# Kernel optimization log

Measured on AMD Instinct MI355X. Metric: run time of the kernel, lower is better.

## Reference

```python
import jax, jax.numpy as jnp
import numpy as np

B, S, D, H = 2, 2048, 2048, 16
HD = D // H  # 128


def _rope(t, cos, sin):
    # t: [B, S, H, HD]; cos/sin: [S, HD//2]
    te, to = t[..., ::2], t[..., 1::2]
    c = cos[None, :, None, :]
    s = sin[None, :, None, :]
    re = te * c - to * s
    im = te * s + to * c
    # interleave back (matches tf.stack(..., axis=-1) + reshape)
    return jnp.stack([re, im], axis=-1).reshape(t.shape)


def setup_inputs() -> dict:
    key = jax.random.key(0)
    ks = jax.random.split(key, 6)
    x = jax.random.normal(ks[0], (B, S, D), dtype=jnp.float32)
    Wq = jax.random.normal(ks[1], (D, D), dtype=jnp.float32) * 0.02
    Wk = jax.random.normal(ks[2], (D, D), dtype=jnp.float32) * 0.02
    Wv = jax.random.normal(ks[3], (D, D), dtype=jnp.float32) * 0.02
    Wo = jax.random.normal(ks[4], (D, D), dtype=jnp.float32) * 0.02
    # rotary embeddings: freqs_cis = exp(i * pos * inv_freq)
    inv_freq = 1.0 / (10000.0 ** (jnp.arange(0, HD, 2, dtype=jnp.float32) / HD))  # [HD//2]
    angles = jnp.arange(S, dtype=jnp.float32)[:, None] * inv_freq[None, :]  # [S, HD//2]
    freqs_cos = jnp.cos(angles)
    freqs_sin = jnp.sin(angles)
    # additive causal mask [1,1,S,S]
    causal = jnp.tril(jnp.ones((S, S), dtype=bool))
    mask = jnp.where(causal, 0.0, -1e9).astype(jnp.float32)[None, None]
    return {"x": x, "Wq": Wq, "Wk": Wk, "Wv": Wv, "Wo": Wo,
            "freqs_cos": freqs_cos, "freqs_sin": freqs_sin, "mask": mask}


def reference(x, Wq, Wk, Wv, Wo, freqs_cos, freqs_sin, mask):
    b, s, d = x.shape
    xq = (x @ Wq).reshape(b, s, H, HD)
    xk = (x @ Wk).reshape(b, s, H, HD)
    xv = (x @ Wv).reshape(b, s, H, HD)
    xq = _rope(xq, freqs_cos, freqs_sin)
    xk = _rope(xk, freqs_cos, freqs_sin)
    # [B, H, S, HD]
    xq = xq.transpose(0, 2, 1, 3)
    xk = xk.transpose(0, 2, 1, 3)
    xv = xv.transpose(0, 2, 1, 3)
    scores = jnp.einsum('bhqd,bhkd->bhqk', xq, xk) / jnp.sqrt(jnp.float32(HD))
    scores = scores + mask[:, :, :s, :s]
    probs = jax.nn.softmax(scores + 1e-9, axis=-1)
    out = jnp.einsum('bhqk,bhkd->bhqd', probs, xv)
    out = out.transpose(0, 2, 1, 3).reshape(b, s, d)
    return out @ Wo
```

## Files before the change

### kernel.cpp

```cpp
#include <hip/hip_runtime.h>
#include <cstdint>

#define BB 2
#define SS 2048
#define DD 2048
#define HH 16
#define HDIM 128
#define MM (BB * SS)

typedef __attribute__((ext_vector_type(8))) short bf16x8;
typedef __attribute__((ext_vector_type(4))) short bf16x4;
typedef __attribute__((ext_vector_type(4))) float f32x4;
typedef __attribute__((ext_vector_type(16))) float f32x16;

__device__ inline short f2bf(float f) {
  union { float f; unsigned u; } v; v.f = f;
  unsigned r = v.u + 0x7FFFu + ((v.u >> 16) & 1u);
  return (short)(r >> 16);
}
__device__ inline float bf2f(short s) {
  union { float f; unsigned u; } v;
  v.u = ((unsigned)(unsigned short)s) << 16;
  return v.f;
}
__device__ inline float asf(int u) { union { int i; float f; } v; v.i = u; return v.f; }
__device__ inline int asi(float f) { union { float f; int i; } v; v.f = f; return v.i; }

__device__ inline unsigned cvtpk_bf16(float lo, float hi) {
  unsigned r;
  asm("v_cvt_pk_bf16_f32 %0, %1, %2" : "=v"(r) : "v"(lo), "v"(hi));
  return r;
}

__device__ inline void gll16(const void* g, void* l) {
  __builtin_amdgcn_global_load_lds(
      (const __attribute__((address_space(1))) void*)g,
      (__attribute__((address_space(3))) void*)l, 16, 0, 0);
}

__global__ __launch_bounds__(256) void cast_bf16_kernel(
    const float* __restrict__ x, short* __restrict__ y, int n4) {
  int i = blockIdx.x * 256 + threadIdx.x;
  if (i >= n4) return;
  float4 v = reinterpret_cast<const float4*>(x)[i];
  bf16x4 o;
  o[0] = f2bf(v.x); o[1] = f2bf(v.y); o[2] = f2bf(v.z); o[3] = f2bf(v.w);
  reinterpret_cast<bf16x4*>(y)[i] = o;
}

__global__ __launch_bounds__(256) void transpose_cast_kernel(
    const float* __restrict__ W, short* __restrict__ Wt) {
  __shared__ short tile[64][65];
  int c = threadIdx.x & 63, r4 = threadIdx.x >> 6;
  int n0 = blockIdx.x << 6, k0 = blockIdx.y << 6;
#pragma unroll
  for (int p = 0; p < 16; ++p) {
    int r = (p << 2) + r4;
    tile[c][r] = f2bf(W[(size_t)(k0 + r) * DD + n0 + c]);
  }
  __syncthreads();
#pragma unroll
  for (int p = 0; p < 16; ++p) {
    int r = (p << 2) + r4;
    Wt[(size_t)(n0 + r) * DD + k0 + c] = tile[r][c];
  }
}

__global__ __launch_bounds__(256) void transpose_v_kernel(
    const short* __restrict__ V, short* __restrict__ Vt) {
  __shared__ short tile[64][65];
  int c = threadIdx.x & 63, r4 = threadIdx.x >> 6;
  int s0 = blockIdx.x << 6, d0 = blockIdx.y << 6;
  int bh = blockIdx.z;
  int b = bh >> 4, h = bh & 15;
#pragma unroll
  for (int p = 0; p < 16; ++p) {
    int r = (p << 2) + r4;
    tile[c][r] = V[(size_t)(b * SS + s0 + r) * DD + h * HDIM + d0 + c];
  }
  __syncthreads();
#pragma unroll
  for (int p = 0; p < 16; ++p) {
    int r = (p << 2) + r4;
    Vt[((size_t)bh * HDIM + d0 + r) * SS + s0 + c] = tile[r][c];
  }
}

__global__ __launch_bounds__(256) void rope_kernel(
    short* __restrict__ Q, short* __restrict__ K,
    const float* __restrict__ fc, const float* __restrict__ fs) {
  int idx = blockIdx.x * 256 + threadIdx.x;
  int m = idx >> 8;
  int c8 = idx & 255;
  int s = m & (SS - 1);
  int i0 = (c8 & 15) << 2;
  const float QS = 0.08838834764831845f;
  float4 c4 = *reinterpret_cast<const float4*>(&fc[s * 64 + i0]);
  float4 s4 = *reinterpret_cast<const float4*>(&fs[s * 64 + i0]);
  float cc[4] = {c4.x, c4.y, c4.z, c4.w};
  float sn[4] = {s4.x, s4.y, s4.z, s4.w};
  size_t off = (size_t)m * DD + (c8 << 3);
  {
    bf16x8 v = *reinterpret_cast<bf16x8*>(&Q[off]);
    bf16x8 o;
#pragma unroll
    for (int p = 0; p < 4; ++p) {
      float e = bf2f(v[2 * p]), od = bf2f(v[2 * p + 1]);
      o[2 * p] = f2bf((e * cc[p] - od * sn[p]) * QS);
      o[2 * p + 1] = f2bf((e * sn[p] + od * cc[p]) * QS);
    }
    *reinterpret_cast<bf16x8*>(&Q[off]) = o;
  }
  {
    bf16x8 v = *reinterpret_cast<bf16x8*>(&K[off]);
    bf16x8 o;
#pragma unroll
    for (int p = 0; p < 4; ++p) {
      float e = bf2f(v[2 * p]), od = bf2f(v[2 * p + 1]);
      o[2 * p] = f2bf(e * cc[p] - od * sn[p]);
      o[2 * p + 1] = f2bf(e * sn[p] + od * cc[p]);
    }
    *reinterpret_cast<bf16x8*>(&K[off]) = o;
  }
}

template <typename OT>
__global__ __launch_bounds__(256) void gemm_kernel(
    const short* __restrict__ A, const short* __restrict__ Bt, OT* __restrict__ C,
    int Mdim, int Ndim, int Kdim) {
  __shared__ short As[128 * 64];
  __shared__ short Bs[128 * 64];
  int tid = threadIdx.x;
  int lane = tid & 63, w = tid >> 6;
  int cl = lane & 15, gq = lane >> 4;
  int wm = w >> 1, wn = w & 1;
  int m0 = blockIdx.y << 7, n0 = blockIdx.x << 7;
  f32x4 acc[4][4];
#pragma unroll
  for (int i = 0; i < 4; ++i)
#pragma unroll
    for (int j = 0; j < 4; ++j) {
      f32x4 z = {0.f, 0.f, 0.f, 0.f};
      acc[i][j] = z;
    }
  int lrow = lane >> 3;
  int lseg = (lane & 7) ^ lrow;

  for (int k0 = 0; k0 < Kdim; k0 += 64) {
#pragma unroll
    for (int i = 0; i < 4; ++i) {
      int r0 = ((w << 2) + i) << 3;
      gll16(&A[(size_t)(m0 + r0 + lrow) * Kdim + k0 + (lseg << 3)], &As[r0 << 6]);
      gll16(&Bt[(size_t)(n0 + r0 + lrow) * Kdim + k0 + (lseg << 3)], &Bs[r0 << 6]);
    }
    __syncthreads();
#pragma unroll
    for (int ks = 0; ks < 2; ++ks) {
      bf16x8 af[4], bfr[4];
#pragma unroll
      for (int f = 0; f < 4; ++f) {
        int ra = (wm << 6) + (f << 4) + cl;
        af[f] = *reinterpret_cast<const bf16x8*>(
            &As[((ra << 6) + (ks << 5) + (gq << 3)) ^ ((ra & 7) << 3)]);
        int rb = (wn << 6) + (f << 4) + cl;
        bfr[f] = *reinterpret_cast<const bf16x8*>(
            &Bs[((rb << 6) + (ks << 5) + (gq << 3)) ^ ((rb & 7) << 3)]);
      }
#pragma unroll
      for (int fm = 0; fm < 4; ++fm)
#pragma unroll
        for (int fn = 0; fn < 4; ++fn)
          acc[fm][fn] = __builtin_amdgcn_mfma_f32_16x16x32_bf16(
              af[fm], bfr[fn], acc[fm][fn], 0, 0, 0);
    }
    __syncthreads();
  }
#pragma unroll
  for (int fm = 0; fm < 4; ++fm)
#pragma unroll
    for (int r = 0; r < 4; ++r) {
      int mrow = m0 + (wm << 6) + (fm << 4) + (gq << 2) + r;
#pragma unroll
      for (int fn = 0; fn < 4; ++fn) {
        int ncol = n0 + (wn << 6) + (fn << 4) + cl;
        float vv = acc[fm][fn][r];
        if constexpr (sizeof(OT) == 2)
          C[(size_t)mrow * Ndim + ncol] = (OT)f2bf(vv);
        else
          C[(size_t)mrow * Ndim + ncol] = vv;
      }
    }
}

__global__ __launch_bounds__(256, 2) void attn_kernel(
    const short* __restrict__ Q, const short* __restrict__ K,
    const short* __restrict__ Vt, short* __restrict__ O) {
  __shared__ short Kl[2][64 * 128];
  __shared__ short Vl[2][128 * 64];
  const int id = blockIdx.x;
  const int qi = 15 - (id >> 5);
  const int bh = id & 31;
  const int b = bh >> 4, h = bh & 15;
  const int tid = threadIdx.x;
  const int lane = tid & 63, w = tid >> 6;
  const int l31 = lane & 31, hi = lane >> 5;
  const int qw = qi * 128 + w * 32;
  const int qg = qw + l31;

  const short* Kbase = K + (size_t)b * SS * DD + h * HDIM;
  const short* Vbase = Vt + (size_t)bh * HDIM * SS;
  int krow[4], kq[4], vd[4], vs[4];
#pragma unroll
  for (int i = 0; i < 4; ++i) {
    int c = w * 4 + i;
    krow[i] = c * 4 + (lane >> 4);
    kq[i] = (lane & 15) ^ (krow[i] & 7);
    vd[i] = c * 8 + (lane >> 3);
    vs[i] = (lane & 7) ^ (vd[i] & 7);
  }

  bf16x8 qf[8];
  const size_t qoff = ((size_t)b * SS + qg) * DD + h * HDIM;
#pragma unroll
  for (int s = 0; s < 8; ++s)
    qf[s] = *reinterpret_cast<const bf16x8*>(&Q[qoff + s * 16 + hi * 8]);

  f32x16 ot[4];
#pragma unroll
  for (int dt = 0; dt < 4; ++dt)
#pragma unroll
    for (int r = 0; r < 16; ++r) ot[dt][r] = 0.f;
  float m_run = -INFINITY, l_run = 0.f;

  const int NT = 2 * qi + 2;

#pragma unroll
  for (int i = 0; i < 4; ++i) {
    gll16(Kbase + (size_t)krow[i] * DD + kq[i] * 8, &Kl[0][(w * 4 + i) * 512]);
    gll16(Vbase + (size_t)vd[i] * SS + vs[i] * 8, &Vl[0][(w * 4 + i) * 512]);
  }
  __syncthreads();

  for (int t = 0; t < NT; ++t) {
    const int cur = t & 1;
    if (t + 1 < NT) {
      const int nt64 = (t + 1) * 64;
#pragma unroll
      for (int i = 0; i < 4; ++i) {
        gll16(Kbase + (size_t)(nt64 + krow[i]) * DD + kq[i] * 8,
              &Kl[cur ^ 1][(w * 4 + i) * 512]);
        gll16(Vbase + (size_t)vd[i] * SS + nt64 + vs[i] * 8,
              &Vl[cur ^ 1][(w * 4 + i) * 512]);
      }
    }

    if (t * 64 <= qw + 31) {
      const short* Kc = Kl[cur];
      const short* Vc = Vl[cur];
      f32x16 st0, st1;
#pragma unroll
      for (int r = 0; r < 16; ++r) { st0[r] = 0.f; st1[r] = 0.f; }
      __builtin_amdgcn_s_setprio(1);
#pragma unroll
      for (int s = 0; s < 8; ++s) {
        const int cs = (s * 2 + hi);
        bf16x8 kf0 = *reinterpret_cast<const bf16x8*>(
            &Kc[l31 * 128 + ((cs ^ (l31 & 7)) << 3)]);
        st0 = __builtin_amdgcn_mfma_f32_32x32x16_bf16(kf0, qf[s], st0, 0, 0, 0);
        bf16x8 kf1 = *reinterpret_cast<const bf16x8*>(
            &Kc[(32 + l31) * 128 + ((cs ^ (l31 & 7)) << 3)]);
        st1 = __builtin_amdgcn_mfma_f32_32x32x16_bf16(kf1, qf[s], st1, 0, 0, 0);
      }
      __builtin_amdgcn_s_setprio(0);
      if (t * 64 + 63 > qw) {
#pragma unroll
        for (int r = 0; r < 16; ++r) {
          int dl = (r & 3) + 8 * (r >> 2) + 4 * hi;
          if (t * 64 + dl > qg) st0[r] = -1e30f;
          if (t * 64 + 32 + dl > qg) st1[r] = -1e30f;
        }
      }
      float pm = st0[0];
#pragma unroll
      for (int r = 1; r < 16; ++r) pm = fmaxf(pm, st0[r]);
#pragma unroll
      for (int r = 0; r < 16; ++r) pm = fmaxf(pm, st1[r]);
      {
        auto sw = __builtin_amdgcn_permlane32_swap(asi(pm), asi(pm), false, false);
        pm = fmaxf(asf(sw[0]), asf(sw[1]));
      }
      if (!__all(pm <= m_run + 8.f)) {
        float mn = fmaxf(m_run, pm);
        float al = __expf(m_run - mn);
        m_run = mn;
        l_run *= al;
#pragma unroll
        for (int dt = 0; dt < 4; ++dt)
#pragma unroll
          for (int r = 0; r < 16; ++r) ot[dt][r] *= al;
      }
      float ps = 0.f;
#pragma unroll
      for (int r = 0; r < 16; ++r) { st0[r] = __expf(st0[r] - m_run); ps += st0[r]; }
#pragma unroll
      for (int r = 0; r < 16; ++r) { st1[r] = __expf(st1[r] - m_run); ps += st1[r]; }
      {
        auto sw = __builtin_amdgcn_permlane32_swap(asi(ps), asi(ps), false, false);
        ps = asf(sw[0]) + asf(sw[1]);
      }
      l_run += ps;

      bf16x8 pf[4];
#pragma unroll
      for (int s = 0; s < 4; ++s) {
        float e0, e1, e2, e3, e4, e5, e6, e7;
        if (s < 2) {
          e0 = st0[8 * s + 0]; e1 = st0[8 * s + 1]; e2 = st0[8 * s + 2]; e3 = st0[8 * s + 3];
          e4 = st0[8 * s + 4]; e5 = st0[8 * s + 5]; e6 = st0[8 * s + 6]; e7 = st0[8 * s + 7];
        } else {
          e0 = st1[8 * (s - 2) + 0]; e1 = st1[8 * (s - 2) + 1]; e2 = st1[8 * (s - 2) + 2]; e3 = st1[8 * (s - 2) + 3];
          e4 = st1[8 * (s - 2) + 4]; e5 = st1[8 * (s - 2) + 5]; e6 = st1[8 * (s - 2) + 6]; e7 = st1[8 * (s - 2) + 7];
        }
        unsigned a0 = cvtpk_bf16(e0, e1);
        unsigned a1 = cvtpk_bf16(e2, e3);
        unsigned b0 = cvtpk_bf16(e4, e5);
        unsigned b1 = cvtpk_bf16(e6, e7);
        auto r0 = __builtin_amdgcn_permlane32_swap((int)a0, (int)b0, false, false);
        auto r1 = __builtin_amdgcn_permlane32_swap((int)a1, (int)b1, false, false);
        union { int u[4]; bf16x8 v; } pk;
        pk.u[0] = r0[0]; pk.u[1] = r1[0]; pk.u[2] = r0[1]; pk.u[3] = r1[1];
        pf[s] = pk.v;
      }

      __builtin_amdgcn_s_setprio(1);
#pragma unroll
      for (int dt = 0; dt < 4; ++dt) {
        const int vr = dt * 32 + l31;
#pragma unroll
        for (int s = 0; s < 4; ++s) {
          bf16x8 vf = *reinterpret_cast<const bf16x8*>(
              &Vc[vr * 64 + (((s * 2 + hi) ^ (vr & 7)) << 3)]);
          ot[dt] = __builtin_amdgcn_mfma_f32_32x32x16_bf16(vf, pf[s], ot[dt], 0, 0, 0);
        }
      }
      __builtin_amdgcn_s_setprio(0);
    }
    __syncthreads();
  }

  float inv = 1.0f / l_run;
  const size_t orow = ((size_t)b * SS + qg) * DD + h * HDIM;
#pragma unroll
  for (int dt = 0; dt < 4; ++dt)
#pragma unroll
    for (int g = 0; g < 4; ++g) {
      bf16x4 v;
#pragma unroll
      for (int k = 0; k < 4; ++k) v[k] = f2bf(ot[dt][4 * g + k] * inv);
      *reinterpret_cast<bf16x4*>(&O[orow + dt * 32 + 8 * g + 4 * hi]) = v;
    }
}

extern "C" void kernel_launch(void* const* d_in, const int* in_sizes, int n_in,
                              void* d_out, int out_size, void* d_ws, size_t ws_size,
                              hipStream_t stream) {
  const float* x = (const float*)d_in[0];
  const float* Wq = (const float*)d_in[1];
  const float* Wk = (const float*)d_in[2];
  const float* Wv = (const float*)d_in[3];
  const float* Wo = (const float*)d_in[4];
  const float* fc = (const float*)d_in[5];
  const float* fs = (const float*)d_in[6];
  float* out = (float*)d_out;
  char* ws = (char*)d_ws;

  short* xb  = (short*)(ws + 0);
  short* WqT = (short*)(ws + (size_t)16 * 1048576);
  short* WkT = (short*)(ws + (size_t)24 * 1048576);
  short* WvT = (short*)(ws + (size_t)32 * 1048576);
  short* WoT = (short*)(ws + (size_t)40 * 1048576);
  short* Qb  = (short*)(ws + (size_t)48 * 1048576);
  short* Kb  = (short*)(ws + (size_t)64 * 1048576);
  short* Vb  = (short*)(ws + (size_t)80 * 1048576);

  cast_bf16_kernel<<<8192, 256, 0, stream>>>(x, xb, 2097152);
  dim3 tg(32, 32);
  transpose_cast_kernel<<<tg, 256, 0, stream>>>(Wq, WqT);
  transpose_cast_kernel<<<tg, 256, 0, stream>>>(Wk, WkT);
  transpose_cast_kernel<<<tg, 256, 0, stream>>>(Wv, WvT);
  transpose_cast_kernel<<<tg, 256, 0, stream>>>(Wo, WoT);

  dim3 gg(16, 32);
  gemm_kernel<short><<<gg, 256, 0, stream>>>(xb, WqT, Qb, MM, DD, DD);
  gemm_kernel<short><<<gg, 256, 0, stream>>>(xb, WkT, Kb, MM, DD, DD);
  gemm_kernel<short><<<gg, 256, 0, stream>>>(xb, WvT, Vb, MM, DD, DD);

  rope_kernel<<<4096, 256, 0, stream>>>(Qb, Kb, fc, fs);
  transpose_v_kernel<<<dim3(32, 2, 32), 256, 0, stream>>>(Vb, xb);

  attn_kernel<<<512, 256, 0, stream>>>(Qb, Kb, xb, Vb);

  gemm_kernel<float><<<gg, 256, 0, stream>>>(Vb, WoT, out, MM, DD, DD);
}
```

Before: 293.5 us.

## Fuse QKV projections with RoPE and V transpose into one GEMM; exp2 softmax

Concatenates Wq/Wk/Wv into one weight buffer and runs a single QKV GEMM whose epilogue applies RoPE (with the softmax scale folded into Q as log2e/sqrt(d)) and writes V already transposed through shared memory. This removes the separate rope and transpose kernels and their round trips through global memory, and fills the grid better with a single 1536-block launch. Attention switches to exp2 and uses tree reductions for the row max and sum, and raises the rescale threshold to 11.5 in the log2 domain, which roughly matches the old threshold of 8.

Measured after the change: 282.6 us. 3.7% less time.

```diff
diff --git a/kernel.cpp b/kernel.cpp
--- a/kernel.cpp
+++ b/kernel.cpp
@@ -66,67 +66,108 @@
   }
 }
 
-__global__ __launch_bounds__(256) void transpose_v_kernel(
-    const short* __restrict__ V, short* __restrict__ Vt) {
-  __shared__ short tile[64][65];
-  int c = threadIdx.x & 63, r4 = threadIdx.x >> 6;
-  int s0 = blockIdx.x << 6, d0 = blockIdx.y << 6;
-  int bh = blockIdx.z;
-  int b = bh >> 4, h = bh & 15;
-#pragma unroll
-  for (int p = 0; p < 16; ++p) {
-    int r = (p << 2) + r4;
-    tile[c][r] = V[(size_t)(b * SS + s0 + r) * DD + h * HDIM + d0 + c];
-  }
-  __syncthreads();
-#pragma unroll
-  for (int p = 0; p < 16; ++p) {
-    int r = (p << 2) + r4;
-    Vt[((size_t)bh * HDIM + d0 + r) * SS + s0 + c] = tile[r][c];
-  }
-}
-
-__global__ __launch_bounds__(256) void rope_kernel(
-    short* __restrict__ Q, short* __restrict__ K,
+__global__ __launch_bounds__(256) void qkv_gemm_kernel(
+    const short* __restrict__ A, const short* __restrict__ Bt,
+    short* __restrict__ Qb, short* __restrict__ Kb, short* __restrict__ Vt,
     const float* __restrict__ fc, const float* __restrict__ fs) {
-  int idx = blockIdx.x * 256 + threadIdx.x;
-  int m = idx >> 8;
-  int c8 = idx & 255;
-  int s = m & (SS - 1);
-  int i0 = (c8 & 15) << 2;
-  const float QS = 0.08838834764831845f;
-  float4 c4 = *reinterpret_cast<const float4*>(&fc[s * 64 + i0]);
-  float4 s4 = *reinterpret_cast<const float4*>(&fs[s * 64 + i0]);
-  float cc[4] = {c4.x, c4.y, c4.z, c4.w};
-  float sn[4] = {s4.x, s4.y, s4.z, s4.w};
-  size_t off = (size_t)m * DD + (c8 << 3);
-  {
-    bf16x8 v = *reinterpret_cast<bf16x8*>(&Q[off]);
-    bf16x8 o;
-#pragma unroll
-    for (int p = 0; p < 4; ++p) {
-      float e = bf2f(v[2 * p]), od = bf2f(v[2 * p + 1]);
-      o[2 * p] = f2bf((e * cc[p] - od * sn[p]) * QS);
-      o[2 * p + 1] = f2bf((e * sn[p] + od * cc[p]) * QS);
-    }
-    *reinterpret_cast<bf16x8*>(&Q[off]) = o;
-  }
-  {
-    bf16x8 v = *reinterpret_cast<bf16x8*>(&K[off]);
-    bf16x8 o;
-#pragma unroll
-    for (int p = 0; p < 4; ++p) {
-      float e = bf2f(v[2 * p]), od = bf2f(v[2 * p + 1]);
-      o[2 * p] = f2bf(e * cc[p] - od * sn[p]);
-      o[2 * p + 1] = f2bf(e * sn[p] + od * cc[p]);
-    }
-    *reinterpret_cast<bf16x8*>(&K[off]) = o;
-  }
-}
-
-template <typename OT>
+  __shared__ short smem[128 * 136];
+  short* As = smem;
+  short* Bs = smem + 8192;
+  const int tid = threadIdx.x;
+  const int lane = tid & 63, w = tid >> 6;
+  const int cl = lane & 15, gq = lane >> 4;
+  const int wm = w >> 1, wn = w & 1;
+  const int m0 = blockIdx.y << 7, n0 = blockIdx.x << 7;
+  const int mat = n0 >> 11;
+  f32x4 acc[4][4];
+#pragma unroll
+  for (int i = 0; i < 4; ++i)
+#pragma unroll
+    for (int j = 0; j < 4; ++j) {
+      f32x4 z = {0.f, 0.f, 0.f, 0.f};
+      acc[i][j] = z;
+    }
+  const int lrow = lane >> 3;
+  const int lseg = (lane & 7) ^ lrow;
+
+  for (int k0 = 0; k0 < DD; k0 += 64) {
+#pragma unroll
+    for (int i = 0; i < 4; ++i) {
+      int r0 = ((w << 2) + i) << 3;
+      gll16(&A[(size_t)(m0 + r0 + lrow) * DD + k0 + (lseg << 3)], &As[r0 << 6]);
+      gll16(&Bt[(size_t)(n0 + r0 + lrow) * DD + k0 + (lseg << 3)], &Bs[r0 << 6]);
+    }
+    __syncthreads();
+#pragma unroll
+    for (int ks = 0; ks < 2; ++ks) {
+      bf16x8 af[4], bfr[4];
+#pragma unroll
+      for (int f = 0; f < 4; ++f) {
+        int ra = (wm << 6) + (f << 4) + cl;
+        af[f] = *reinterpret_cast<const bf16x8*>(
+            &As[((ra << 6) + (ks << 5) + (gq << 3)) ^ ((ra & 7) << 3)]);
+        int rb = (wn << 6) + (f << 4) + cl;
+        bfr[f] = *reinterpret_cast<const bf16x8*>(
+            &Bs[((rb << 6) + (ks << 5) + (gq << 3)) ^ ((rb & 7) << 3)]);
+      }
+#pragma unroll
+      for (int fm = 0; fm < 4; ++fm)
+#pragma unroll
+        for (int fn = 0; fn < 4; ++fn)
+          acc[fm][fn] = __builtin_amdgcn_mfma_f32_16x16x32_bf16(
+              af[fm], bfr[fn], acc[fm][fn], 0, 0, 0);
+    }
+    __syncthreads();
+  }
+
+  if (mat < 2) {
+    const float qs = (mat == 0) ? 0.127517448f : 1.0f;
+    short* Dst = (mat == 0) ? Qb : Kb;
+#pragma unroll
+    for (int fm = 0; fm < 4; ++fm)
+#pragma unroll
+      for (int r = 0; r < 4; ++r) {
+        int mrow = m0 + (wm << 6) + (fm << 4) + (gq << 2) + r;
+        int s = mrow & (SS - 1);
+#pragma unroll
+        for (int fn = 0; fn < 4; ++fn) {
+          int c = (wn << 6) + (fn << 4) + cl;
+          int i = c >> 1;
+          float cv = fc[s * 64 + i], sv = fs[s * 64 + i];
+          float v = acc[fm][fn][r];
+          float vp = __shfl_xor(v, 1, 64);
+          float out = (c & 1) ? (v * cv + vp * sv) : (v * cv - vp * sv);
+          Dst[(size_t)mrow * DD + ((n0 + c) & (DD - 1))] = f2bf(out * qs);
+        }
+      }
+  } else {
+    short* Tt = smem;
+#pragma unroll
+    for (int fm = 0; fm < 4; ++fm)
+#pragma unroll
+      for (int fn = 0; fn < 4; ++fn) {
+        int c = (wn << 6) + (fn << 4) + cl;
+        int rb = (wm << 6) + (fm << 4) + (gq << 2);
+        bf16x4 v4;
+#pragma unroll
+        for (int rr = 0; rr < 4; ++rr) v4[rr] = f2bf(acc[fm][fn][rr]);
+        *reinterpret_cast<bf16x4*>(&Tt[c * 136 + rb]) = v4;
+      }
+    __syncthreads();
+    int d = tid >> 1, half = tid & 1;
+    int bq = m0 >> 11, s0loc = m0 & (SS - 1);
+    int hv = (n0 >> 7) - 32;
+    size_t vb = (((size_t)(bq * 16 + hv) * HDIM + d) * SS) + s0loc + half * 64;
+#pragma unroll
+    for (int j = 0; j < 8; ++j) {
+      bf16x8 v = *reinterpret_cast<const bf16x8*>(&Tt[d * 136 + half * 64 + j * 8]);
+      *reinterpret_cast<bf16x8*>(&Vt[vb + j * 8]) = v;
+    }
+  }
+}
+
 __global__ __launch_bounds__(256) void gemm_kernel(
-    const short* __restrict__ A, const short* __restrict__ Bt, OT* __restrict__ C,
+    const short* __restrict__ A, const short* __restrict__ Bt, float* __restrict__ C,
     int Mdim, int Ndim, int Kdim) {
   __shared__ short As[128 * 64];
   __shared__ short Bs[128 * 64];
@@ -183,11 +224,7 @@
 #pragma unroll
       for (int fn = 0; fn < 4; ++fn) {
         int ncol = n0 + (wn << 6) + (fn << 4) + cl;
-        float vv = acc[fm][fn][r];
-        if constexpr (sizeof(OT) == 2)
-          C[(size_t)mrow * Ndim + ncol] = (OT)f2bf(vv);
-        else
-          C[(size_t)mrow * Ndim + ncol] = vv;
+        C[(size_t)mrow * Ndim + ncol] = acc[fm][fn][r];
       }
     }
 }
@@ -280,18 +317,22 @@
           if (t * 64 + 32 + dl > qg) st1[r] = -1e30f;
         }
       }
-      float pm = st0[0];
-#pragma unroll
-      for (int r = 1; r < 16; ++r) pm = fmaxf(pm, st0[r]);
-#pragma unroll
-      for (int r = 0; r < 16; ++r) pm = fmaxf(pm, st1[r]);
+      float mx[16];
+#pragma unroll
+      for (int r = 0; r < 16; ++r) mx[r] = fmaxf(st0[r], st1[r]);
+#pragma unroll
+      for (int off = 8; off >= 1; off >>= 1)
+#pragma unroll
+        for (int r = 0; r < 8; ++r)
+          if (r < off) mx[r] = fmaxf(mx[r], mx[r + off]);
+      float pm = mx[0];
       {
         auto sw = __builtin_amdgcn_permlane32_swap(asi(pm), asi(pm), false, false);
         pm = fmaxf(asf(sw[0]), asf(sw[1]));
       }
-      if (!__all(pm <= m_run + 8.f)) {
+      if (!__all(pm <= m_run + 11.5f)) {
         float mn = fmaxf(m_run, pm);
-        float al = __expf(m_run - mn);
+        float al = exp2f(m_run - mn);
         m_run = mn;
         l_run *= al;
 #pragma unroll
@@ -299,11 +340,19 @@
 #pragma unroll
           for (int r = 0; r < 16; ++r) ot[dt][r] *= al;
       }
-      float ps = 0.f;
-#pragma unroll
-      for (int r = 0; r < 16; ++r) { st0[r] = __expf(st0[r] - m_run); ps += st0[r]; }
-#pragma unroll
-      for (int r = 0; r < 16; ++r) { st1[r] = __expf(st1[r] - m_run); ps += st1[r]; }
+#pragma unroll
+      for (int r = 0; r < 16; ++r) st0[r] = exp2f(st0[r] - m_run);
+#pragma unroll
+      for (int r = 0; r < 16; ++r) st1[r] = exp2f(st1[r] - m_run);
+      float sm[16];
+#pragma unroll
+      for (int r = 0; r < 16; ++r) sm[r] = st0[r] + st1[r];
+#pragma unroll
+      for (int off = 8; off >= 1; off >>= 1)
+#pragma unroll
+        for (int r = 0; r < 8; ++r)
+          if (r < off) sm[r] += sm[r + off];
+      float ps = sm[0];
       {
         auto sw = __builtin_amdgcn_permlane32_swap(asi(ps), asi(ps), false, false);
         ps = asf(sw[0]) + asf(sw[1]);
@@ -374,31 +423,23 @@
   float* out = (float*)d_out;
   char* ws = (char*)d_ws;
 
-  short* xb  = (short*)(ws + 0);
-  short* WqT = (short*)(ws + (size_t)16 * 1048576);
-  short* WkT = (short*)(ws + (size_t)24 * 1048576);
-  short* WvT = (short*)(ws + (size_t)32 * 1048576);
-  short* WoT = (short*)(ws + (size_t)40 * 1048576);
-  short* Qb  = (short*)(ws + (size_t)48 * 1048576);
-  short* Kb  = (short*)(ws + (size_t)64 * 1048576);
-  short* Vb  = (short*)(ws + (size_t)80 * 1048576);
+  short* xb     = (short*)(ws + 0);
+  short* WqkvT  = (short*)(ws + (size_t)16 * 1048576);
+  short* WoT    = (short*)(ws + (size_t)40 * 1048576);
+  short* Qb     = (short*)(ws + (size_t)48 * 1048576);
+  short* Kb     = (short*)(ws + (size_t)64 * 1048576);
+  short* VtB    = (short*)(ws + (size_t)80 * 1048576);
 
   cast_bf16_kernel<<<8192, 256, 0, stream>>>(x, xb, 2097152);
   dim3 tg(32, 32);
-  transpose_cast_kernel<<<tg, 256, 0, stream>>>(Wq, WqT);
-  transpose_cast_kernel<<<tg, 256, 0, stream>>>(Wk, WkT);
-  transpose_cast_kernel<<<tg, 256, 0, stream>>>(Wv, WvT);
+  transpose_cast_kernel<<<tg, 256, 0, stream>>>(Wq, WqkvT);
+  transpose_cast_kernel<<<tg, 256, 0, stream>>>(Wk, WqkvT + (size_t)2048 * 2048);
+  transpose_cast_kernel<<<tg, 256, 0, stream>>>(Wv, WqkvT + (size_t)4096 * 2048);
   transpose_cast_kernel<<<tg, 256, 0, stream>>>(Wo, WoT);
 
-  dim3 gg(16, 32);
-  gemm_kernel<short><<<gg, 256, 0, stream>>>(xb, WqT, Qb, MM, DD, DD);
-  gemm_kernel<short><<<gg, 256, 0, stream>>>(xb, WkT, Kb, MM, DD, DD);
-  gemm_kernel<short><<<gg, 256, 0, stream>>>(xb, WvT, Vb, MM, DD, DD);
-
-  rope_kernel<<<4096, 256, 0, stream>>>(Qb, Kb, fc, fs);
-  transpose_v_kernel<<<dim3(32, 2, 32), 256, 0, stream>>>(Vb, xb);
-
-  attn_kernel<<<512, 256, 0, stream>>>(Qb, Kb, xb, Vb);
-
-  gemm_kernel<float><<<gg, 256, 0, stream>>>(Vb, WoT, out, MM, DD, DD);
-}
+  qkv_gemm_kernel<<<dim3(48, 32), 256, 0, stream>>>(xb, WqkvT, Qb, Kb, VtB, fc, fs);
+
+  attn_kernel<<<512, 256, 0, stream>>>(Qb, Kb, VtB, xb);
+
+  gemm_kernel<<<dim3(16, 32), 256, 0, stream>>>(xb, WoT, out, MM, DD, DD);
+}
```
